# Performance work log

Measured on AMD Instinct MI355X. Metric: run time of the kernel, lower is better.

## Reference

```python
import jax, jax.numpy as jnp
import numpy as np

B = 65536          # bs * m
N_NODES = 2        # fixed by module usage (job-machine pair graphs)
IN_FEAT = 256
N_HEADS = 4
N_HIDDEN = 256     # concat=False -> n_hidden = out_features
SLOPE = 0.2


def setup_inputs() -> dict:
    key = jax.random.key(0)
    k_h, k_adj, k_w, k_a = jax.random.split(key, 4)
    h = jax.random.normal(k_h, (B, N_NODES, IN_FEAT), dtype=jnp.float32)
    # adjacency: ij=1 means edge j->i; force self-loops on the diagonal
    adj = jax.random.randint(k_adj, (B, 1, N_NODES, N_NODES), 0, 2, dtype=jnp.int32)
    diag = jnp.arange(N_NODES)
    adj = adj.at[..., diag, diag].set(1)
    # xavier-normal-ish scales
    W = jax.random.normal(k_w, (IN_FEAT, N_HIDDEN * N_HEADS), dtype=jnp.float32) * (2.0 / (IN_FEAT + N_HIDDEN * N_HEADS)) ** 0.5
    a = jax.random.normal(k_a, (N_HEADS, 2 * N_HIDDEN, 1), dtype=jnp.float32) * (2.0 / (2 * N_HIDDEN + 1)) ** 0.5
    return {"h": h, "adj_mat": adj, "W": W, "a": a}


def reference(h, adj_mat, W, a):
    # h: (B, N, F_in); W: (F_in, H*D); a: (H, 2D, 1); adj_mat: (B, 1, N, N)
    Bsz, n_nodes, _ = h.shape
    n_heads = a.shape[0]
    n_hidden = a.shape[1] // 2
    # (B, N, H*D) -> (B, H, N, D)
    ht = (h @ W).reshape(Bsz, n_nodes, n_heads, n_hidden).transpose(0, 2, 1, 3)
    # attention scores: e[b,h,i,j] = leakyrelu(src[b,h,i] + tgt[b,h,j])
    src = jnp.einsum('bhnd,hd->bhn', ht, a[:, :n_hidden, 0])
    tgt = jnp.einsum('bhnd,hd->bhn', ht, a[:, n_hidden:, 0])
    e = jax.nn.leaky_relu(src[..., :, None] + tgt[..., None, :], SLOPE)
    e = jnp.where(adj_mat > 0, e, -jnp.inf)  # (B, H, N, N)
    attn = jax.nn.softmax(e, axis=-1)
    h_prime = jnp.einsum('bhij,bhjd->bhid', attn, ht)  # (B, H, N, D)
    # concat=False -> mean over heads
    return h_prime.mean(axis=1)  # (B, N, D)
```

## Files before the change

kernel.cpp:

```cpp
#include <hip/hip_runtime.h>
#include <hip/hip_bf16.h>


typedef __attribute__((ext_vector_type(8))) short short8;
typedef __attribute__((ext_vector_type(4))) float floatx4;

__device__ __forceinline__ float bf2f(short u) {
    union { unsigned int i; float f; } v;
    v.i = ((unsigned int)(unsigned short)u) << 16;
    return v.f;
}
__device__ __forceinline__ unsigned int pk2(float lo, float hi) {
    __hip_bfloat162 t = __float22bfloat162_rn(make_float2(lo, hi));
    union { __hip_bfloat162 h; unsigned int u; } cv; cv.h = t;
    return cv.u;
}

__global__ void gat_prep(const float* __restrict__ W, const float* __restrict__ a,
                         __hip_bfloat16* __restrict__ PT,
                         __hip_bfloat16* __restrict__ Wt2) {
    int b = blockIdx.x;
    if (b < 1024) {
        int idx = b * 256 + threadIdx.x;
        int d = idx & 255, hh = (idx >> 8) & 3, k = idx >> 10;
        int j = k >> 5, kl = k & 31;
        Wt2[(((hh * 8 + j) * 256 + d) << 5) + kl] =
            __float2bfloat16(W[k * 1024 + hh * 256 + d]);
    } else {
        int wid = (b - 1024) * 4 + (threadIdx.x >> 6);
        int lane = threadIdx.x & 63;
        int k = wid & 255, h = (wid >> 8) & 3, half = wid >> 10;
        float4 wv = *(const float4*)(W + k * 1024 + h * 256 + lane * 4);
        float4 av = *(const float4*)(a + h * 512 + half * 256 + lane * 4);
        float s = wv.x * av.x + wv.y * av.y + wv.z * av.z + wv.w * av.w;
        #pragma unroll
        for (int off = 32; off; off >>= 1) s += __shfl_down(s, off);
        if (lane == 0) PT[(half * 4 + h) * 256 + k] = __float2bfloat16(s);
        if (lane == 1) PT[2048 + wid] = __float2bfloat16(0.f);
    }
}

#define TB 32
#define ROWS 64
#define HS 264
#define ZS 136

__global__ __launch_bounds__(256, 3)
void gat_main(const float* __restrict__ hin,
              const int* __restrict__ adj,
              const __hip_bfloat16* __restrict__ PT,
              const __hip_bfloat16* __restrict__ Wt2,
              float* __restrict__ out) {
    __shared__ __align__(16) __hip_bfloat16 sH[ROWS][HS];
    __shared__ __align__(16) unsigned char uZ[ROWS * ZS * 2];
    __shared__ __align__(16) float2 sC[TB * 4 * 2];
    __hip_bfloat16 (*sZ)[ZS]  = (__hip_bfloat16 (*)[ZS])uZ;
    __hip_bfloat16 (*sPT)[HS] = (__hip_bfloat16 (*)[HS])uZ;
    float (*sS)[16] = (float (*)[16])(uZ + 8448);

    const int tid = threadIdx.x;
    const int lane = tid & 63;
    const int wave = tid >> 6;
    const int m = lane & 15;
    const int q = lane >> 4;
    const long batch0 = (long)blockIdx.x * TB;

    #pragma unroll
    for (int it = 0; it < 2; ++it) {
        int idx = tid + it * 256;
        int n = idx >> 5, cg = idx & 31;
        int4 v = ((const int4*)PT)[idx];
        *(int4*)&sPT[n][cg * 8] = v;
    }
    {
        const float4* gh = (const float4*)(hin + batch0 * 512);
        #pragma unroll
        for (int it = 0; it < 16; ++it) {
            int idx = tid + it * 256;
            int r = idx >> 6, c4 = idx & 63;
            float4 v = gh[idx];
            uint2 bv;
            bv.x = pk2(v.x, v.y);
            bv.y = pk2(v.z, v.w);
            *(uint2*)&sH[r][c4 * 4] = bv;
        }
    }
    __syncthreads();

    {
        floatx4 a0 = {0.f, 0.f, 0.f, 0.f};
        #pragma unroll
        for (int ks = 0; ks < 8; ++ks) {
            short8 bf = *(const short8*)&sPT[m][ks * 32 + q * 8];
            short8 f0 = *(const short8*)&sH[wave * 16 + m][ks * 32 + q * 8];
            a0 = __builtin_amdgcn_mfma_f32_16x16x32_bf16(f0, bf, a0, 0, 0, 0);
        }
        #pragma unroll
        for (int r = 0; r < 4; ++r)
            sS[wave * 16 + q * 4 + r][m] = a0[r];
    }
    __syncthreads();

    {
        int lb = tid >> 3, hh = (tid >> 1) & 3, i = tid & 1;
        int4 av = ((const int4*)adj)[batch0 + lb];
        int m0 = i ? av.z : av.x, m1 = i ? av.w : av.y;
        float s  = sS[lb * 2 + i][hh];
        float t0 = sS[lb * 2][4 + hh], t1 = sS[lb * 2 + 1][4 + hh];
        float e0 = s + t0; e0 = e0 >= 0.f ? e0 : 0.2f * e0;
        float e1 = s + t1; e1 = e1 >= 0.f ? e1 : 0.2f * e1;
        e0 = fminf(fmaxf(e0, -80.f), 80.f);
        e1 = fminf(fmaxf(e1, -80.f), 80.f);
        bool k0 = m0 > 0, k1 = m1 > 0;
        float f0 = k0 ? e0 : -1e30f, f1 = k1 ? e1 : -1e30f;
        float mx = fmaxf(f0, f1);
        float p0 = k0 ? __expf(e0 - mx) : 0.f;
        float p1 = k1 ? __expf(e1 - mx) : 0.f;
        float den = p0 + p1;
        float inv = den > 1e-30f ? 0.25f / den : 0.f;
        sC[(lb * 4 + hh) * 2 + i] = make_float2(p0 * inv, p1 * inv);
    }

    floatx4 acc[4][4];
    #pragma unroll
    for (int i = 0; i < 4; ++i)
        #pragma unroll
        for (int j = 0; j < 4; ++j)
            acc[i][j] = (floatx4){0.f, 0.f, 0.f, 0.f};

    #pragma unroll 1
    for (int hh = 0; hh < 4; ++hh) {
        #pragma unroll 1
        for (int s = 0; s < 2; ++s) {
            __syncthreads();
            {
                int g = tid & 15, rb = tid >> 4;
                #pragma unroll
                for (int it = 0; it < 4; ++it) {
                    int zr = rb + it * 16;
                    float2 c = sC[((zr >> 1) * 4 + hh) * 2 + (zr & 1)];
                    int hr = zr & ~1;
                    short8 v0 = *(const short8*)&sH[hr][s * 128 + g * 8];
                    short8 v1 = *(const short8*)&sH[hr + 1][s * 128 + g * 8];
                    int4 zv; int* zp = (int*)&zv;
                    #pragma unroll
                    for (int jj = 0; jj < 4; ++jj) {
                        float z0 = c.x * bf2f(v0[jj * 2])     + c.y * bf2f(v1[jj * 2]);
                        float z1 = c.x * bf2f(v0[jj * 2 + 1]) + c.y * bf2f(v1[jj * 2 + 1]);
                        zp[jj] = (int)pk2(z0, z1);
                    }
                    *(int4*)&sZ[zr][g * 8] = zv;
                }
            }
            __syncthreads();
            #pragma unroll
            for (int js = 0; js < 4; ++js) {
                int jg = hh * 8 + s * 4 + js;
                const short* wb = (const short*)Wt2 +
                                  ((jg * 256 + wave * 64 + m) << 5) + q * 8;
                short8 bfr[4];
                #pragma unroll
                for (int nt = 0; nt < 4; ++nt)
                    bfr[nt] = *(const short8*)(wb + nt * 512);
                #pragma unroll
                for (int mt = 0; mt < 4; ++mt) {
                    short8 af = *(const short8*)&sZ[mt * 16 + m][js * 32 + q * 8];
                    #pragma unroll
                    for (int nt = 0; nt < 4; ++nt)
                        acc[mt][nt] = __builtin_amdgcn_mfma_f32_16x16x32_bf16(
                            af, bfr[nt], acc[mt][nt], 0, 0, 0);
                }
            }
        }
    }

    {
        float* og = out + batch0 * 512;
        #pragma unroll
        for (int mt = 0; mt < 4; ++mt)
            #pragma unroll
            for (int nt = 0; nt < 4; ++nt) {
                int col = wave * 64 + nt * 16 + m;
                #pragma unroll
                for (int r = 0; r < 4; ++r)
                    og[(mt * 16 + q * 4 + r) * 256 + col] = acc[mt][nt][r];
            }
    }
}

extern "C" void kernel_launch(void* const* d_in, const int* in_sizes, int n_in,
                              void* d_out, int out_size, void* d_ws, size_t ws_size,
                              hipStream_t stream) {
    const float* hin = (const float*)d_in[0];
    const int* adj   = (const int*)d_in[1];
    const float* W   = (const float*)d_in[2];
    const float* a   = (const float*)d_in[3];
    float* out       = (float*)d_out;

    __hip_bfloat16* PT  = (__hip_bfloat16*)d_ws;
    __hip_bfloat16* Wt2 = PT + 16 * 256;

    if (ws_size < (16 * 256 + 256 * 1024) * sizeof(__hip_bfloat16)) return;

    int B = in_sizes[0] / 512;
    gat_prep<<<1536, 256, 0, stream>>>(W, a, PT, Wt2);
    gat_main<<<B / TB, 256, 0, stream>>>(hin, adj, PT, Wt2, out);
}
```

Measured before the change: 293.4 us.

## Build attention-mixed A fragments in registers and retile waves to 2x2

The main loop no longer stages the attention-weighted Z tile through shared memory with two barriers per head/half step. Each wave now computes its MFMA A fragments directly in registers from XOR-swizzled bf16 rows of h, using attention coefficients preloaded per row. Waves are retiled as a 2x2 grid (32 rows x 128 cols), which halves the A work per wave but doubles the W fragments each wave loads. The PT projection is read straight from global memory instead of shared, and the adjacency load is issued early. This removes most of the barriers and LDS round trips, at the cost of more register pressure and recomputing the mixes per column half.

Result: slower. 402.5 us (+37.2%).

```diff
diff --git a/kernel.cpp b/kernel.cpp
--- a/kernel.cpp
+++ b/kernel.cpp
@@ -42,8 +42,6 @@
 
 #define TB 32
 #define ROWS 64
-#define HS 264
-#define ZS 136
 
 __global__ __launch_bounds__(256, 3)
 void gat_main(const float* __restrict__ hin,
@@ -51,12 +49,9 @@
               const __hip_bfloat16* __restrict__ PT,
               const __hip_bfloat16* __restrict__ Wt2,
               float* __restrict__ out) {
-    __shared__ __align__(16) __hip_bfloat16 sH[ROWS][HS];
-    __shared__ __align__(16) unsigned char uZ[ROWS * ZS * 2];
+    __shared__ __align__(16) short sH[ROWS * 256];
+    __shared__ __align__(16) float sS[ROWS][16];
     __shared__ __align__(16) float2 sC[TB * 4 * 2];
-    __hip_bfloat16 (*sZ)[ZS]  = (__hip_bfloat16 (*)[ZS])uZ;
-    __hip_bfloat16 (*sPT)[HS] = (__hip_bfloat16 (*)[HS])uZ;
-    float (*sS)[16] = (float (*)[16])(uZ + 8448);
 
     const int tid = threadIdx.x;
     const int lane = tid & 63;
@@ -64,14 +59,10 @@
     const int m = lane & 15;
     const int q = lane >> 4;
     const long batch0 = (long)blockIdx.x * TB;
-
-    #pragma unroll
-    for (int it = 0; it < 2; ++it) {
-        int idx = tid + it * 256;
-        int n = idx >> 5, cg = idx & 31;
-        int4 v = ((const int4*)PT)[idx];
-        *(int4*)&sPT[n][cg * 8] = v;
-    }
+    char* sHb = (char*)sH;
+
+    int4 av = ((const int4*)adj)[batch0 + (tid >> 3)];
+
     {
         const float4* gh = (const float4*)(hin + batch0 * 512);
         #pragma unroll
@@ -82,17 +73,20 @@
             uint2 bv;
             bv.x = pk2(v.x, v.y);
             bv.y = pk2(v.z, v.w);
-            *(uint2*)&sH[r][c4 * 4] = bv;
+            *(uint2*)(sHb + r * 512 + ((c4 * 8) ^ ((r & 7) << 4))) = bv;
         }
     }
     __syncthreads();
 
     {
+        const short* ptg = (const short*)PT;
+        int row = wave * 16 + m;
         floatx4 a0 = {0.f, 0.f, 0.f, 0.f};
         #pragma unroll
         for (int ks = 0; ks < 8; ++ks) {
-            short8 bf = *(const short8*)&sPT[m][ks * 32 + q * 8];
-            short8 f0 = *(const short8*)&sH[wave * 16 + m][ks * 32 + q * 8];
+            short8 bf = *(const short8*)(ptg + m * 256 + ks * 32 + q * 8);
+            short8 f0 = *(const short8*)(sHb + row * 512 +
+                          ((ks * 64 + q * 16) ^ ((row & 7) << 4)));
             a0 = __builtin_amdgcn_mfma_f32_16x16x32_bf16(f0, bf, a0, 0, 0, 0);
         }
         #pragma unroll
@@ -103,7 +97,6 @@
 
     {
         int lb = tid >> 3, hh = (tid >> 1) & 3, i = tid & 1;
-        int4 av = ((const int4*)adj)[batch0 + lb];
         int m0 = i ? av.z : av.x, m1 = i ? av.w : av.y;
         float s  = sS[lb * 2 + i][hh];
         float t0 = sS[lb * 2][4 + hh], t1 = sS[lb * 2 + 1][4 + hh];
@@ -120,70 +113,82 @@
         float inv = den > 1e-30f ? 0.25f / den : 0.f;
         sC[(lb * 4 + hh) * 2 + i] = make_float2(p0 * inv, p1 * inv);
     }
-
-    floatx4 acc[4][4];
+    __syncthreads();
+
+    const int wr = wave >> 1, wc = wave & 1;
+
+    float2 c2[2][4];
     #pragma unroll
-    for (int i = 0; i < 4; ++i)
-        #pragma unroll
-        for (int j = 0; j < 4; ++j)
+    for (int mt = 0; mt < 2; ++mt)
+        #pragma unroll
+        for (int hh = 0; hh < 4; ++hh) {
+            int zr = wr * 32 + mt * 16 + m;
+            c2[mt][hh] = sC[((zr >> 1) * 4 + hh) * 2 + (zr & 1)];
+        }
+
+    floatx4 acc[2][8];
+    #pragma unroll
+    for (int i = 0; i < 2; ++i)
+        #pragma unroll
+        for (int j = 0; j < 8; ++j)
             acc[i][j] = (floatx4){0.f, 0.f, 0.f, 0.f};
 
     #pragma unroll 1
-    for (int hh = 0; hh < 4; ++hh) {
-        #pragma unroll 1
-        for (int s = 0; s < 2; ++s) {
-            __syncthreads();
-            {
-                int g = tid & 15, rb = tid >> 4;
-                #pragma unroll
-                for (int it = 0; it < 4; ++it) {
-                    int zr = rb + it * 16;
-                    float2 c = sC[((zr >> 1) * 4 + hh) * 2 + (zr & 1)];
-                    int hr = zr & ~1;
-                    short8 v0 = *(const short8*)&sH[hr][s * 128 + g * 8];
-                    short8 v1 = *(const short8*)&sH[hr + 1][s * 128 + g * 8];
-                    int4 zv; int* zp = (int*)&zv;
+    for (int js = 0; js < 8; ++js) {
+        short8 v0[2], v1[2];
+        #pragma unroll
+        for (int mt = 0; mt < 2; ++mt) {
+            int hr = wr * 32 + mt * 16 + (m & ~1);
+            int co = js * 64 + q * 16;
+            v0[mt] = *(const short8*)(sHb + hr * 512 + (co ^ ((hr & 7) << 4)));
+            v1[mt] = *(const short8*)(sHb + (hr + 1) * 512 + (co ^ (((hr + 1) & 7) << 4)));
+        }
+        float f0[2][8], f1[2][8];
+        #pragma unroll
+        for (int mt = 0; mt < 2; ++mt)
+            #pragma unroll
+            for (int e = 0; e < 8; ++e) {
+                f0[mt][e] = bf2f(v0[mt][e]);
+                f1[mt][e] = bf2f(v1[mt][e]);
+            }
+        #pragma unroll
+        for (int hh = 0; hh < 4; ++hh) {
+            union { short8 s; unsigned int u[4]; } fr[2];
+            #pragma unroll
+            for (int mt = 0; mt < 2; ++mt)
+                #pragma unroll
+                for (int p = 0; p < 4; ++p) {
+                    float z0 = c2[mt][hh].x * f0[mt][p * 2]     + c2[mt][hh].y * f1[mt][p * 2];
+                    float z1 = c2[mt][hh].x * f0[mt][p * 2 + 1] + c2[mt][hh].y * f1[mt][p * 2 + 1];
+                    fr[mt].u[p] = pk2(z0, z1);
+                }
+            const short* wbase = (const short*)Wt2 + (((hh * 8 + js) * 256 + wc * 128) << 5);
+            #pragma unroll
+            for (int ntg = 0; ntg < 2; ++ntg) {
+                short8 bfr[4];
+                #pragma unroll
+                for (int nt = 0; nt < 4; ++nt)
+                    bfr[nt] = *(const short8*)(wbase + (((ntg * 4 + nt) * 16 + m) << 5) + q * 8);
+                #pragma unroll
+                for (int nt = 0; nt < 4; ++nt)
                     #pragma unroll
-                    for (int jj = 0; jj < 4; ++jj) {
-                        float z0 = c.x * bf2f(v0[jj * 2])     + c.y * bf2f(v1[jj * 2]);
-                        float z1 = c.x * bf2f(v0[jj * 2 + 1]) + c.y * bf2f(v1[jj * 2 + 1]);
-                        zp[jj] = (int)pk2(z0, z1);
-                    }
-                    *(int4*)&sZ[zr][g * 8] = zv;
-                }
+                    for (int mt = 0; mt < 2; ++mt)
+                        acc[mt][ntg * 4 + nt] = __builtin_amdgcn_mfma_f32_16x16x32_bf16(
+                            fr[mt].s, bfr[nt], acc[mt][ntg * 4 + nt], 0, 0, 0);
             }
-            __syncthreads();
-            #pragma unroll
-            for (int js = 0; js < 4; ++js) {
-                int jg = hh * 8 + s * 4 + js;
-                const short* wb = (const short*)Wt2 +
-                                  ((jg * 256 + wave * 64 + m) << 5) + q * 8;
-                short8 bfr[4];
-                #pragma unroll
-                for (int nt = 0; nt < 4; ++nt)
-                    bfr[nt] = *(const short8*)(wb + nt * 512);
-                #pragma unroll
-                for (int mt = 0; mt < 4; ++mt) {
-                    short8 af = *(const short8*)&sZ[mt * 16 + m][js * 32 + q * 8];
-                    #pragma unroll
-                    for (int nt = 0; nt < 4; ++nt)
-                        acc[mt][nt] = __builtin_amdgcn_mfma_f32_16x16x32_bf16(
-                            af, bfr[nt], acc[mt][nt], 0, 0, 0);
-                }
-            }
         }
     }
 
     {
         float* og = out + batch0 * 512;
         #pragma unroll
-        for (int mt = 0; mt < 4; ++mt)
-            #pragma unroll
-            for (int nt = 0; nt < 4; ++nt) {
-                int col = wave * 64 + nt * 16 + m;
+        for (int mt = 0; mt < 2; ++mt)
+            #pragma unroll
+            for (int nt = 0; nt < 8; ++nt) {
+                int col = wc * 128 + nt * 16 + m;
                 #pragma unroll
                 for (int r = 0; r < 4; ++r)
-                    og[(mt * 16 + q * 4 + r) * 256 + col] = acc[mt][nt][r];
+                    og[(wr * 32 + mt * 16 + q * 4 + r) * 256 + col] = acc[mt][nt][r];
             }
     }
 }
```

## Double-buffer Z tiles with XOR-swizzled LDS and register-held PT fragments

Applied to the files above, without the earlier changes.

Replaces the padded LDS layouts with XOR-swizzled unpadded layouts for both the h tile and the attention-weighted Z tile. The Z buffer is split into two 64-column buffers, and the loop now runs over 16 chunks with one barrier each: it builds the next chunk while running MFMAs on the current one. PT fragments and the adjacency row are loaded straight into registers early instead of going through LDS. The aim is fewer barriers and bank conflicts and better overlap of VALU and MFMA work, at the cost of more registers and more complicated indexing.

Measured after the change: 291.3 us. No clear change (-0.7%).

```diff
diff --git a/kernel.cpp b/kernel.cpp
--- a/kernel.cpp
+++ b/kernel.cpp
@@ -42,8 +42,6 @@
 
 #define TB 32
 #define ROWS 64
-#define HS 264
-#define ZS 136
 
 __global__ __launch_bounds__(256, 3)
 void gat_main(const float* __restrict__ hin,
@@ -51,12 +49,10 @@
               const __hip_bfloat16* __restrict__ PT,
               const __hip_bfloat16* __restrict__ Wt2,
               float* __restrict__ out) {
-    __shared__ __align__(16) __hip_bfloat16 sH[ROWS][HS];
-    __shared__ __align__(16) unsigned char uZ[ROWS * ZS * 2];
+    __shared__ __align__(16) short sH[ROWS * 256];
+    __shared__ __align__(16) short sZd[2][ROWS * 64];
     __shared__ __align__(16) float2 sC[TB * 4 * 2];
-    __hip_bfloat16 (*sZ)[ZS]  = (__hip_bfloat16 (*)[ZS])uZ;
-    __hip_bfloat16 (*sPT)[HS] = (__hip_bfloat16 (*)[HS])uZ;
-    float (*sS)[16] = (float (*)[16])(uZ + 8448);
+    float (*sS)[16] = (float (*)[16])(&sZd[1][0]);
 
     const int tid = threadIdx.x;
     const int lane = tid & 63;
@@ -64,14 +60,18 @@
     const int m = lane & 15;
     const int q = lane >> 4;
     const long batch0 = (long)blockIdx.x * TB;
-
-    #pragma unroll
-    for (int it = 0; it < 2; ++it) {
-        int idx = tid + it * 256;
-        int n = idx >> 5, cg = idx & 31;
-        int4 v = ((const int4*)PT)[idx];
-        *(int4*)&sPT[n][cg * 8] = v;
-    }
+    char* sHb = (char*)sH;
+    char* sZb = (char*)sZd;
+
+    short8 ptf[8];
+    {
+        const short* ptg = (const short*)PT;
+        #pragma unroll
+        for (int ks = 0; ks < 8; ++ks)
+            ptf[ks] = *(const short8*)(ptg + m * 256 + ks * 32 + q * 8);
+    }
+    int4 av = ((const int4*)adj)[batch0 + (tid >> 3)];
+
     {
         const float4* gh = (const float4*)(hin + batch0 * 512);
         #pragma unroll
@@ -82,18 +82,19 @@
             uint2 bv;
             bv.x = pk2(v.x, v.y);
             bv.y = pk2(v.z, v.w);
-            *(uint2*)&sH[r][c4 * 4] = bv;
+            *(uint2*)(sHb + r * 512 + ((c4 * 8) ^ ((r & 7) << 4))) = bv;
         }
     }
     __syncthreads();
 
     {
+        int row = wave * 16 + m;
         floatx4 a0 = {0.f, 0.f, 0.f, 0.f};
         #pragma unroll
         for (int ks = 0; ks < 8; ++ks) {
-            short8 bf = *(const short8*)&sPT[m][ks * 32 + q * 8];
-            short8 f0 = *(const short8*)&sH[wave * 16 + m][ks * 32 + q * 8];
-            a0 = __builtin_amdgcn_mfma_f32_16x16x32_bf16(f0, bf, a0, 0, 0, 0);
+            short8 f0 = *(const short8*)(sHb + row * 512 +
+                          ((ks * 64 + q * 16) ^ ((row & 7) << 4)));
+            a0 = __builtin_amdgcn_mfma_f32_16x16x32_bf16(f0, ptf[ks], a0, 0, 0, 0);
         }
         #pragma unroll
         for (int r = 0; r < 4; ++r)
@@ -103,7 +104,6 @@
 
     {
         int lb = tid >> 3, hh = (tid >> 1) & 3, i = tid & 1;
-        int4 av = ((const int4*)adj)[batch0 + lb];
         int m0 = i ? av.z : av.x, m1 = i ? av.w : av.y;
         float s  = sS[lb * 2 + i][hh];
         float t0 = sS[lb * 2][4 + hh], t1 = sS[lb * 2 + 1][4 + hh];
@@ -120,6 +120,31 @@
         float inv = den > 1e-30f ? 0.25f / den : 0.f;
         sC[(lb * 4 + hh) * 2 + i] = make_float2(p0 * inv, p1 * inv);
     }
+    __syncthreads();
+
+    const int zg = tid & 7, zrb = tid >> 3;
+
+    #define ZBUILD(ch, buf)                                                     \
+    {                                                                           \
+        int hh_ = (ch) >> 2, kc_ = (ch) & 3;                                    \
+        _Pragma("unroll")                                                       \
+        for (int half = 0; half < 2; ++half) {                                  \
+            int zr = zrb + half * 32;                                           \
+            float2 c = sC[((zr >> 1) * 4 + hh_) * 2 + (zr & 1)];                \
+            int hr = zr & ~1;                                                   \
+            int co = kc_ * 128 + zg * 16;                                       \
+            short8 v0 = *(const short8*)(sHb + hr * 512 + (co ^ ((hr & 7) << 4))); \
+            short8 v1 = *(const short8*)(sHb + (hr + 1) * 512 + (co ^ (((hr + 1) & 7) << 4))); \
+            int4 zv; int* zp = (int*)&zv;                                       \
+            _Pragma("unroll")                                                   \
+            for (int jj = 0; jj < 4; ++jj) {                                    \
+                float z0 = c.x * bf2f(v0[jj * 2])     + c.y * bf2f(v1[jj * 2]); \
+                float z1 = c.x * bf2f(v0[jj * 2 + 1]) + c.y * bf2f(v1[jj * 2 + 1]); \
+                zp[jj] = (int)pk2(z0, z1);                                      \
+            }                                                                   \
+            *(int4*)(sZb + (buf) * 8192 + zr * 128 + ((zg * 16) ^ ((zr & 7) << 4))) = zv; \
+        }                                                                       \
+    }
 
     floatx4 acc[4][4];
     #pragma unroll
@@ -128,50 +153,39 @@
         for (int j = 0; j < 4; ++j)
             acc[i][j] = (floatx4){0.f, 0.f, 0.f, 0.f};
 
+    ZBUILD(0, 0);
+    __syncthreads();
+
+    int cur = 0;
     #pragma unroll 1
-    for (int hh = 0; hh < 4; ++hh) {
-        #pragma unroll 1
-        for (int s = 0; s < 2; ++s) {
-            __syncthreads();
-            {
-                int g = tid & 15, rb = tid >> 4;
-                #pragma unroll
-                for (int it = 0; it < 4; ++it) {
-                    int zr = rb + it * 16;
-                    float2 c = sC[((zr >> 1) * 4 + hh) * 2 + (zr & 1)];
-                    int hr = zr & ~1;
-                    short8 v0 = *(const short8*)&sH[hr][s * 128 + g * 8];
-                    short8 v1 = *(const short8*)&sH[hr + 1][s * 128 + g * 8];
-                    int4 zv; int* zp = (int*)&zv;
-                    #pragma unroll
-                    for (int jj = 0; jj < 4; ++jj) {
-                        float z0 = c.x * bf2f(v0[jj * 2])     + c.y * bf2f(v1[jj * 2]);
-                        float z1 = c.x * bf2f(v0[jj * 2 + 1]) + c.y * bf2f(v1[jj * 2 + 1]);
-                        zp[jj] = (int)pk2(z0, z1);
-                    }
-                    *(int4*)&sZ[zr][g * 8] = zv;
-                }
-            }
-            __syncthreads();
+    for (int ch = 0; ch < 16; ++ch) {
+        short8 bfr[2][4];
+        {
+            int hh = ch >> 2, kc = ch & 3;
             #pragma unroll
-            for (int js = 0; js < 4; ++js) {
-                int jg = hh * 8 + s * 4 + js;
+            for (int ks = 0; ks < 2; ++ks) {
                 const short* wb = (const short*)Wt2 +
-                                  ((jg * 256 + wave * 64 + m) << 5) + q * 8;
-                short8 bfr[4];
+                    (((hh * 8 + kc * 2 + ks) * 256 + wave * 64 + m) << 5) + q * 8;
                 #pragma unroll
                 for (int nt = 0; nt < 4; ++nt)
-                    bfr[nt] = *(const short8*)(wb + nt * 512);
-                #pragma unroll
-                for (int mt = 0; mt < 4; ++mt) {
-                    short8 af = *(const short8*)&sZ[mt * 16 + m][js * 32 + q * 8];
-                    #pragma unroll
-                    for (int nt = 0; nt < 4; ++nt)
-                        acc[mt][nt] = __builtin_amdgcn_mfma_f32_16x16x32_bf16(
-                            af, bfr[nt], acc[mt][nt], 0, 0, 0);
-                }
+                    bfr[ks][nt] = *(const short8*)(wb + (nt << 9));
             }
         }
+        if (ch < 15) ZBUILD(ch + 1, cur ^ 1);
+        #pragma unroll
+        for (int ks = 0; ks < 2; ++ks)
+            #pragma unroll
+            for (int mt = 0; mt < 4; ++mt) {
+                int row = mt * 16 + m;
+                short8 af = *(const short8*)(sZb + cur * 8192 + row * 128 +
+                              ((ks * 64 + q * 16) ^ ((row & 7) << 4)));
+                #pragma unroll
+                for (int nt = 0; nt < 4; ++nt)
+                    acc[mt][nt] = __builtin_amdgcn_mfma_f32_16x16x32_bf16(
+                        af, bfr[ks][nt], acc[mt][nt], 0, 0, 0);
+            }
+        __syncthreads();
+        cur ^= 1;
     }
 
     {
@@ -186,6 +200,7 @@
                     og[(mt * 16 + q * 4 + r) * 256 + col] = acc[mt][nt][r];
             }
     }
+    #undef ZBUILD
 }
 
 extern "C" void kernel_launch(void* const* d_in, const int* in_sizes, int n_in,
```
